# Optimization experiments

Measured on AMD Instinct MI355X. Metric: run time of the kernel, lower is better.

Reference implementation:

```python
import jax, jax.numpy as jnp
import numpy as np

EPS = 1e-9
TEMP = 1.0
TOP_K = 2


def setup_inputs() -> dict:
    key = jax.random.key(0)
    k1, k2, k3, k4 = jax.random.split(key, 4)
    B, T, D, DC, E = 8, 4096, 1024, 512, 64
    din = D + DC
    inputs = jax.random.normal(k1, (B, T, D), dtype=jnp.float32)
    cond = jax.random.normal(k2, (B, T, DC), dtype=jnp.float32)
    # CondRouterMLP params (bias=False): Linear(din -> 2*din), GELU, Linear(2*din -> E)
    W1 = jax.random.normal(k3, (2 * din, din), dtype=jnp.float32) / np.sqrt(din).astype(np.float32)
    W2 = jax.random.normal(k4, (E, 2 * din), dtype=jnp.float32) / np.sqrt(2 * din).astype(np.float32)
    return {"inputs": inputs, "cond": cond, "W1": W1, "W2": W2}


def reference(inputs, cond, W1, W2):
    B, T, D = inputs.shape
    # concat hidden states with condition, flatten tokens
    x = jnp.concatenate([inputs, cond], axis=-1).reshape(-1, D + cond.shape[-1])  # [N, din]
    h = jax.nn.gelu(x @ W1.T, approximate=False)          # [N, 2*din] (torch nn.GELU = exact erf)
    logits = h @ W2.T                                     # [N, E]
    logits = (logits - logits.max(axis=-1, keepdims=True)) / TEMP
    probs = jax.nn.softmax(logits, axis=-1) + EPS
    probs = jnp.clip(probs, EPS, 1.0 - EPS)               # [N, E]
    # eval-mode top-k selection
    top_v, top_i = jax.lax.top_k(probs, TOP_K)            # [N, k]
    N, E = probs.shape
    rows = jnp.arange(N)[:, None]
    router_mask = jnp.zeros_like(probs).at[rows, top_i].set(1.0)
    router_probs = jnp.zeros_like(probs).at[rows, top_i].set(top_v)
    router_probs = router_probs / router_probs.sum(axis=-1, keepdims=True)  # normalize=True
    return (
        router_mask.reshape(B, T, E),
        top_i.reshape(B, T, TOP_K),
        router_probs.reshape(B, T, E),
        probs.reshape(B, T, E),
    )
```

## Files before the change

### kernel.cpp

```cpp
#include <hip/hip_runtime.h>
#include <cmath>

#define N_TOK 32768
#define D0    1024
#define DCC   512
#define DIN   1536
#define JD    3072
#define NE    64
#define BM    128
#define BJ    256
#define BK    32
#define NJC   (JD/BJ)
#define NIT   (DIN/BK)
#define NTH   512
#define HS    36
#define EPSV  1e-9f

typedef _Float16 half8 __attribute__((ext_vector_type(8)));
typedef float    f32x4 __attribute__((ext_vector_type(4)));

#define SZ_A  16384
#define SZ_B  32768
#define OFF_A 0
#define OFF_B 32768
#define LDS_TOTAL 98304
#define OFF_H    0
#define OFF_LRED 0
#define OFF_EPI  36864

#define W1T_G (192*3072)
#define W2T_G (384*64)

__device__ __forceinline__ f32x4 mfma16(half8 a, half8 b, f32x4 c) {
    return __builtin_amdgcn_mfma_f32_16x16x32_f16(a, b, c, 0, 0, 0);
}

__device__ __forceinline__ void split8(const float4 v0, const float4 v1, half8& hh, half8& hl) {
    float f[8] = {v0.x, v0.y, v0.z, v0.w, v1.x, v1.y, v1.z, v1.w};
    #pragma unroll
    for (int i = 0; i < 8; ++i) {
        _Float16 h = (_Float16)f[i];
        hh[i] = h;
        hl[i] = (_Float16)(f[i] - (float)h);
    }
}

__device__ __forceinline__ void gload16(const void* g, void* l) {
    __builtin_amdgcn_global_load_lds(
        (const __attribute__((address_space(1))) unsigned int*)g,
        (__attribute__((address_space(3))) unsigned int*)l, 16, 0, 0);
}

__global__ void presplit_w1t(const float* __restrict__ W1,
                             _Float16* __restrict__ hi, _Float16* __restrict__ lo) {
    int g = blockIdx.x * blockDim.x + threadIdx.x;
    if (g >= W1T_G) return;
    const int j  = g % JD;
    const int ko = g / JD;
    const float* src = W1 + (size_t)j * DIN + ko * 8;
    float4 v0 = *(const float4*)src;
    float4 v1 = *(const float4*)(src + 4);
    half8 h, l;
    split8(v0, v1, h, l);
    *(half8*)(hi + (size_t)g * 8) = h;
    *(half8*)(lo + (size_t)g * 8) = l;
}

__global__ void presplit_w2t(const float* __restrict__ W2,
                             _Float16* __restrict__ hi, _Float16* __restrict__ lo) {
    int g = blockIdx.x * blockDim.x + threadIdx.x;
    if (g >= W2T_G) return;
    const int e  = g & 63;
    const int jo = g >> 6;
    const float* src = W2 + (size_t)e * JD + jo * 8;
    float4 v0 = *(const float4*)src;
    float4 v1 = *(const float4*)(src + 4);
    half8 h, l;
    split8(v0, v1, h, l);
    *(half8*)(hi + (size_t)g * 8) = h;
    *(half8*)(lo + (size_t)g * 8) = l;
}

__global__ __launch_bounds__(NTH, 1)
void router_v9(const float* __restrict__ inp, const float* __restrict__ cnd,
               const _Float16* __restrict__ W1h, const _Float16* __restrict__ W1l,
               const _Float16* __restrict__ W2h, const _Float16* __restrict__ W2l,
               float* __restrict__ out_mask, float* __restrict__ out_topi,
               float* __restrict__ out_rp, float* __restrict__ out_probs)
{
    __shared__ __align__(16) char smem[LDS_TOTAL];

    const int tid  = threadIdx.x;
    const int lane = tid & 63;
    const int w    = tid >> 6;
    const int tg   = w >> 2;
    const int jg   = w & 3;
    const int l15  = lane & 15;
    const int lg   = lane >> 4;
    const int t0   = blockIdx.x * BM;

    const int akoct = w >> 1;
    const int arow  = (w & 1) * 64 + lane;
    const int bplane = w >> 2;
    const int bkoct  = w & 3;

    int aoff[4], boff[4];
    #pragma unroll
    for (int tf = 0; tf < 4; ++tf) aoff[tf] = (lg*128 + tg*64 + tf*16 + l15) * 16;
    #pragma unroll
    for (int jf = 0; jf < 4; ++jf) boff[jf] = (lg*256 + jg*64 + jf*16 + l15) * 16;

    const f32x4 vzero = {0.f, 0.f, 0.f, 0.f};
    f32x4 lacc[4] = {vzero, vzero, vzero, vzero};

    const float* const xrowA = inp + (size_t)(t0 + arow) * D0;
    const float* const xrowC = cnd + (size_t)(t0 + arow) * DCC;
    const _Float16* const Wbp = bplane ? W1l : W1h;

    _Float16* const myHh = (_Float16*)(smem + OFF_H + w * 9216);
    _Float16* const myHl = myHh + 2304;

    for (int jc = 0; jc < NJC; ++jc) {
        f32x4 acc1[4][4];
        #pragma unroll
        for (int tf = 0; tf < 4; ++tf)
            #pragma unroll
            for (int jf = 0; jf < 4; ++jf) acc1[tf][jf] = vzero;

        {
            #pragma unroll
            for (int q = 0; q < 4; ++q) {
                const _Float16* src = Wbp + ((size_t)bkoct * JD + jc*BJ + q*64 + lane) * 8;
                char* dst = smem + OFF_B + bplane*16384 + bkoct*4096 + q*1024;
                gload16(src, dst);
            }
            const float* sx = xrowA + akoct * 8;
            float4 v0 = *(const float4*)sx;
            float4 v1 = *(const float4*)(sx + 4);
            half8 hh, hl;
            split8(v0, v1, hh, hl);
            const int g = (akoct*128 + arow) * 16;
            *(half8*)(smem + OFF_A + g) = hh;
            *(half8*)(smem + OFF_A + 8192 + g) = hl;
        }
        __syncthreads();

        for (int it = 0; it < NIT; ++it) {
            const int cur = it & 1, nxt = cur ^ 1;
            const bool more = (it + 1 < NIT);
            float4 xv0, xv1;
            if (more) {
                const int ko = (it + 1) * 4 + bkoct;
                #pragma unroll
                for (int q = 0; q < 4; ++q) {
                    const _Float16* src = Wbp + ((size_t)ko * JD + jc*BJ + q*64 + lane) * 8;
                    char* dst = smem + OFF_B + nxt*SZ_B + bplane*16384 + bkoct*4096 + q*1024;
                    gload16(src, dst);
                }
                const int k = (it + 1) * BK + akoct * 8;
                const float* sx = (k < D0) ? (xrowA + k) : (xrowC + k - D0);
                xv0 = *(const float4*)sx;
                xv1 = *(const float4*)(sx + 4);
            }
            const char* ab = smem + OFF_A + cur*SZ_A;
            const char* bb = smem + OFF_B + cur*SZ_B;
            half8 ah[4], al[4], bh[4], bl[4];
            #pragma unroll
            for (int tf = 0; tf < 4; ++tf) {
                ah[tf] = *(const half8*)(ab + aoff[tf]);
                al[tf] = *(const half8*)(ab + 8192 + aoff[tf]);
            }
            #pragma unroll
            for (int jf = 0; jf < 4; ++jf) {
                bh[jf] = *(const half8*)(bb + boff[jf]);
                bl[jf] = *(const half8*)(bb + 16384 + boff[jf]);
            }
            #pragma unroll
            for (int tf = 0; tf < 4; ++tf)
                #pragma unroll
                for (int jf = 0; jf < 4; ++jf) {
                    acc1[tf][jf] = mfma16(ah[tf], bh[jf], acc1[tf][jf]);
                    acc1[tf][jf] = mfma16(ah[tf], bl[jf], acc1[tf][jf]);
                    acc1[tf][jf] = mfma16(al[tf], bh[jf], acc1[tf][jf]);
                }
            if (more) {
                half8 hh, hl;
                split8(xv0, xv1, hh, hl);
                const int g = (akoct*128 + arow) * 16;
                *(half8*)(smem + OFF_A + nxt*SZ_A + g) = hh;
                *(half8*)(smem + OFF_A + nxt*SZ_A + 8192 + g) = hl;
            }
            __syncthreads();
        }

        #pragma unroll
        for (int r = 0; r < 2; ++r) {
            #pragma unroll
            for (int c = 0; c < 2; ++c) {
                const int jf = 2*r + c;
                #pragma unroll
                for (int tf = 0; tf < 4; ++tf)
                    #pragma unroll
                    for (int rr = 0; rr < 4; ++rr) {
                        const float v = acc1[tf][jf][rr];
                        const float gv = 0.5f * v * (1.0f + erff(v * 0.70710678118654752f));
                        const _Float16 gh = (_Float16)gv;
                        const _Float16 gl = (_Float16)(gv - (float)gh);
                        const int o = (tf*16 + lg*4 + rr) * HS + c*16 + l15;
                        myHh[o] = gh; myHl[o] = gl;
                    }
            }
            __syncthreads();
            #pragma unroll
            for (int s = 0; s < 4; ++s) {
                const _Float16* sh = (const _Float16*)(smem + OFF_H + (tg*4 + s) * 9216);
                const _Float16* sl = sh + 2304;
                const int jo = jc*32 + s*8 + r*4 + lg;
                const size_t wg = ((size_t)jo * 64 + jg*16 + l15) * 8;
                half8 b2h = *(const half8*)(W2h + wg);
                half8 b2l = *(const half8*)(W2l + wg);
                #pragma unroll
                for (int tf = 0; tf < 4; ++tf) {
                    const int o = (tf*16 + l15) * HS + lg*8;
                    half8 a2h = *(const half8*)(sh + o);
                    half8 a2l = *(const half8*)(sl + o);
                    lacc[tf] = mfma16(a2h, b2h, lacc[tf]);
                    lacc[tf] = mfma16(a2h, b2l, lacc[tf]);
                    lacc[tf] = mfma16(a2l, b2h, lacc[tf]);
                }
            }
            __syncthreads();
        }
    }

    float* const Lred = (float*)(smem + OFF_LRED);
    #pragma unroll
    for (int tf = 0; tf < 4; ++tf)
        #pragma unroll
        for (int rr = 0; rr < 4; ++rr)
            Lred[(tg*64 + tf*16 + lg*4 + rr) * 68 + jg*16 + l15] = lacc[tf][rr];
    __syncthreads();

    float* const mA   = (float*)(smem + OFF_EPI);
    float* const invA = mA + BM;
    int*   const i1A  = (int*)(invA + BM);
    int*   const i2A  = i1A + BM;
    float* const rp1A = (float*)(i2A + BM);
    float* const rp2A = rp1A + BM;

    if (tid < BM) {
        const float* row = Lred + tid * 68;
        float m = -3.402823466e38f;
        for (int e = 0; e < NE; ++e) m = fmaxf(m, row[e]);
        float s = 0.f, v1 = -3.402823466e38f, v2 = -3.402823466e38f;
        int i1 = 0, i2 = 0;
        for (int e = 0; e < NE; ++e) {
            const float v = row[e];
            s += expf(v - m);
            if (v > v1)      { v2 = v1; i2 = i1; v1 = v; i1 = e; }
            else if (v > v2) { v2 = v; i2 = e; }
        }
        const float inv = 1.f / s;
        const float p1 = fminf(expf(v1 - m) * inv + EPSV, 1.f - EPSV);
        const float p2 = fminf(expf(v2 - m) * inv + EPSV, 1.f - EPSV);
        mA[tid] = m; invA[tid] = inv; i1A[tid] = i1; i2A[tid] = i2;
        const float den = p1 + p2;
        rp1A[tid] = p1 / den; rp2A[tid] = p2 / den;
    }
    __syncthreads();

    for (int idx = tid; idx < BM * NE; idx += NTH) {
        const int r = idx >> 6, e = idx & 63;
        const size_t o = (size_t)(t0 + r) * NE + e;
        const float p = fminf(expf(Lred[r * 68 + e] - mA[r]) * invA[r] + EPSV, 1.f - EPSV);
        const int b1 = (e == i1A[r]), b2 = (e == i2A[r]);
        out_probs[o] = p;
        out_mask[o]  = (b1 | b2) ? 1.f : 0.f;
        out_rp[o]    = b1 ? rp1A[r] : (b2 ? rp2A[r] : 0.f);
    }
    if (tid < BM * 2) {
        const int r = tid >> 1, q = tid & 1;
        out_topi[(size_t)(t0 + r) * 2 + q] = (float)(q ? i2A[r] : i1A[r]);
    }
}

extern "C" void kernel_launch(void* const* d_in, const int* in_sizes, int n_in,
                              void* d_out, int out_size, void* d_ws, size_t ws_size,
                              hipStream_t stream) {
    const float* inp = (const float*)d_in[0];
    const float* cnd = (const float*)d_in[1];
    const float* W1  = (const float*)d_in[2];
    const float* W2  = (const float*)d_in[3];

    float* out = (float*)d_out;
    const size_t NT = (size_t)N_TOK;
    float* out_mask  = out;
    float* out_topi  = out + NT * NE;
    float* out_rp    = out + NT * NE + NT * 2;
    float* out_probs = out + NT * NE + NT * 2 + NT * NE;

    _Float16* W1h = (_Float16*)d_ws;
    _Float16* W1l = W1h + (size_t)W1T_G * 8;
    _Float16* W2h = W1l + (size_t)W1T_G * 8;
    _Float16* W2l = W2h + (size_t)W2T_G * 8;

    hipLaunchKernelGGL(presplit_w1t, dim3((W1T_G + 255) / 256), dim3(256), 0, stream, W1, W1h, W1l);
    hipLaunchKernelGGL(presplit_w2t, dim3((W2T_G + 255) / 256), dim3(256), 0, stream, W2, W2h, W2l);
    hipLaunchKernelGGL(router_v9, dim3(N_TOK / BM), dim3(NTH), 0, stream,
                       inp, cnd, W1h, W1l, W2h, W2l,
                       out_mask, out_topi, out_rp, out_probs);
}
```

Baseline: 1.098 ms.

## Halve token tile, load A fragments directly into registers, pipeline W1 across chunks

Cuts the block to 64 tokens and 4 waves so two blocks can share a CU. Each wave now reads its activation rows straight from global memory into MFMA fragments and splits them to hi/lo fp16 in registers, so the A tile is no longer staged in LDS. The W1 prefetch now runs across j-chunk boundaries, removing the per-chunk prologue sync. The cost is that every W1 tile is re-streamed for half as many tokens, which doubles W1 traffic, and the uncoalesced per-lane row loads of x may raise global load latency.

```diff
diff --git a/kernel.cpp b/kernel.cpp
--- a/kernel.cpp
+++ b/kernel.cpp
@@ -7,26 +7,22 @@
 #define DIN   1536
 #define JD    3072
 #define NE    64
-#define BM    128
+#define BM    64
 #define BJ    256
 #define BK    32
 #define NJC   (JD/BJ)
 #define NIT   (DIN/BK)
-#define NTH   512
-#define HS    36
+#define NTH   256
 #define EPSV  1e-9f
 
 typedef _Float16 half8 __attribute__((ext_vector_type(8)));
 typedef float    f32x4 __attribute__((ext_vector_type(4)));
 
-#define SZ_A  16384
 #define SZ_B  32768
-#define OFF_A 0
-#define OFF_B 32768
-#define LDS_TOTAL 98304
-#define OFF_H    0
+#define LDS_TOTAL 65536
+#define OFF_H 32768
 #define OFF_LRED 0
-#define OFF_EPI  36864
+#define OFF_EPI  18432
 
 #define W1T_G (192*3072)
 #define W2T_G (384*64)
@@ -81,152 +77,153 @@
     *(half8*)(lo + (size_t)g * 8) = l;
 }
 
-__global__ __launch_bounds__(NTH, 1)
-void router_v9(const float* __restrict__ inp, const float* __restrict__ cnd,
-               const _Float16* __restrict__ W1h, const _Float16* __restrict__ W1l,
-               const _Float16* __restrict__ W2h, const _Float16* __restrict__ W2l,
-               float* __restrict__ out_mask, float* __restrict__ out_topi,
-               float* __restrict__ out_rp, float* __restrict__ out_probs)
+__global__ __launch_bounds__(NTH, 2)
+void router_v10(const float* __restrict__ inp, const float* __restrict__ cnd,
+                const _Float16* __restrict__ W1h, const _Float16* __restrict__ W1l,
+                const _Float16* __restrict__ W2h, const _Float16* __restrict__ W2l,
+                float* __restrict__ out_mask, float* __restrict__ out_topi,
+                float* __restrict__ out_rp, float* __restrict__ out_probs)
 {
     __shared__ __align__(16) char smem[LDS_TOTAL];
 
     const int tid  = threadIdx.x;
     const int lane = tid & 63;
     const int w    = tid >> 6;
-    const int tg   = w >> 2;
-    const int jg   = w & 3;
+    const int tg   = w >> 1;
+    const int jg   = w & 1;
     const int l15  = lane & 15;
     const int lg   = lane >> 4;
     const int t0   = blockIdx.x * BM;
 
-    const int akoct = w >> 1;
-    const int arow  = (w & 1) * 64 + lane;
-    const int bplane = w >> 2;
-    const int bkoct  = w & 3;
-
-    int aoff[4], boff[4];
+    const int spl = w >> 1;
+    const int sko = (w & 1) * 2;
+
+    int boff[8];
     #pragma unroll
-    for (int tf = 0; tf < 4; ++tf) aoff[tf] = (lg*128 + tg*64 + tf*16 + l15) * 16;
+    for (int jf = 0; jf < 8; ++jf)
+        boff[jf] = (lg * 256 + jg * 128 + jf * 16 + l15) * 16;
+
+    const float* pA[2];
+    const float* pC[2];
     #pragma unroll
-    for (int jf = 0; jf < 4; ++jf) boff[jf] = (lg*256 + jg*64 + jf*16 + l15) * 16;
+    for (int tf = 0; tf < 2; ++tf) {
+        const int row = t0 + tg * 32 + tf * 16 + l15;
+        pA[tf] = inp + (size_t)row * D0;
+        pC[tf] = cnd + (size_t)row * DCC;
+    }
+
+    _Float16* const myHh = (_Float16*)(smem + OFF_H + w * 4608);
+    _Float16* const myHl = myHh + 1152;
 
     const f32x4 vzero = {0.f, 0.f, 0.f, 0.f};
     f32x4 lacc[4] = {vzero, vzero, vzero, vzero};
 
-    const float* const xrowA = inp + (size_t)(t0 + arow) * D0;
-    const float* const xrowC = cnd + (size_t)(t0 + arow) * DCC;
-    const _Float16* const Wbp = bplane ? W1l : W1h;
-
-    _Float16* const myHh = (_Float16*)(smem + OFF_H + w * 9216);
-    _Float16* const myHl = myHh + 2304;
+    float4 xv[2][2];
+    {
+        #pragma unroll
+        for (int d = 0; d < 2; ++d) {
+            const int ko = sko + d;
+            #pragma unroll
+            for (int q = 0; q < 4; ++q) {
+                const _Float16* src = (spl ? W1l : W1h) +
+                    ((size_t)ko * JD + q * 64 + lane) * 8;
+                gload16(src, smem + ((spl * 4 + ko) * 256 + q * 64) * 16);
+            }
+        }
+        #pragma unroll
+        for (int tf = 0; tf < 2; ++tf) {
+            const float* s = pA[tf] + lg * 8;
+            xv[tf][0] = *(const float4*)s;
+            xv[tf][1] = *(const float4*)(s + 4);
+        }
+    }
+    __syncthreads();
 
     for (int jc = 0; jc < NJC; ++jc) {
-        f32x4 acc1[4][4];
-        #pragma unroll
-        for (int tf = 0; tf < 4; ++tf)
-            #pragma unroll
-            for (int jf = 0; jf < 4; ++jf) acc1[tf][jf] = vzero;
-
-        {
-            #pragma unroll
-            for (int q = 0; q < 4; ++q) {
-                const _Float16* src = Wbp + ((size_t)bkoct * JD + jc*BJ + q*64 + lane) * 8;
-                char* dst = smem + OFF_B + bplane*16384 + bkoct*4096 + q*1024;
-                gload16(src, dst);
-            }
-            const float* sx = xrowA + akoct * 8;
-            float4 v0 = *(const float4*)sx;
-            float4 v1 = *(const float4*)(sx + 4);
-            half8 hh, hl;
-            split8(v0, v1, hh, hl);
-            const int g = (akoct*128 + arow) * 16;
-            *(half8*)(smem + OFF_A + g) = hh;
-            *(half8*)(smem + OFF_A + 8192 + g) = hl;
-        }
-        __syncthreads();
+        f32x4 acc1[2][8];
+        #pragma unroll
+        for (int tf = 0; tf < 2; ++tf)
+            #pragma unroll
+            for (int jf = 0; jf < 8; ++jf) acc1[tf][jf] = vzero;
 
         for (int it = 0; it < NIT; ++it) {
-            const int cur = it & 1, nxt = cur ^ 1;
-            const bool more = (it + 1 < NIT);
-            float4 xv0, xv1;
+            const int cur = it & 1;
+            const bool more = !(jc == NJC - 1 && it == NIT - 1);
+            half8 ah[2], al[2];
+            #pragma unroll
+            for (int tf = 0; tf < 2; ++tf)
+                split8(xv[tf][0], xv[tf][1], ah[tf], al[tf]);
             if (more) {
-                const int ko = (it + 1) * 4 + bkoct;
-                #pragma unroll
-                for (int q = 0; q < 4; ++q) {
-                    const _Float16* src = Wbp + ((size_t)ko * JD + jc*BJ + q*64 + lane) * 8;
-                    char* dst = smem + OFF_B + nxt*SZ_B + bplane*16384 + bkoct*4096 + q*1024;
-                    gload16(src, dst);
+                const int itn = (it == NIT - 1) ? 0 : it + 1;
+                const int jcn = (it == NIT - 1) ? jc + 1 : jc;
+                char* bb = smem + (cur ^ 1) * SZ_B;
+                #pragma unroll
+                for (int d = 0; d < 2; ++d) {
+                    const int ko = sko + d;
+                    const size_t kog = (size_t)(itn * 4 + ko) * JD + jcn * BJ;
+                    #pragma unroll
+                    for (int q = 0; q < 4; ++q) {
+                        const _Float16* src = (spl ? W1l : W1h) + (kog + q * 64 + lane) * 8;
+                        gload16(src, bb + ((spl * 4 + ko) * 256 + q * 64) * 16);
+                    }
                 }
-                const int k = (it + 1) * BK + akoct * 8;
-                const float* sx = (k < D0) ? (xrowA + k) : (xrowC + k - D0);
-                xv0 = *(const float4*)sx;
-                xv1 = *(const float4*)(sx + 4);
-            }
-            const char* ab = smem + OFF_A + cur*SZ_A;
-            const char* bb = smem + OFF_B + cur*SZ_B;
-            half8 ah[4], al[4], bh[4], bl[4];
-            #pragma unroll
-            for (int tf = 0; tf < 4; ++tf) {
-                ah[tf] = *(const half8*)(ab + aoff[tf]);
-                al[tf] = *(const half8*)(ab + 8192 + aoff[tf]);
-            }
-            #pragma unroll
-            for (int jf = 0; jf < 4; ++jf) {
-                bh[jf] = *(const half8*)(bb + boff[jf]);
-                bl[jf] = *(const half8*)(bb + 16384 + boff[jf]);
-            }
-            #pragma unroll
-            for (int tf = 0; tf < 4; ++tf)
-                #pragma unroll
-                for (int jf = 0; jf < 4; ++jf) {
-                    acc1[tf][jf] = mfma16(ah[tf], bh[jf], acc1[tf][jf]);
-                    acc1[tf][jf] = mfma16(ah[tf], bl[jf], acc1[tf][jf]);
-                    acc1[tf][jf] = mfma16(al[tf], bh[jf], acc1[tf][jf]);
+                const int k0 = itn * BK + lg * 8;
+                #pragma unroll
+                for (int tf = 0; tf < 2; ++tf) {
+                    const float* s = (itn < 32) ? (pA[tf] + k0) : (pC[tf] + k0 - D0);
+                    xv[tf][0] = *(const float4*)s;
+                    xv[tf][1] = *(const float4*)(s + 4);
                 }
-            if (more) {
-                half8 hh, hl;
-                split8(xv0, xv1, hh, hl);
-                const int g = (akoct*128 + arow) * 16;
-                *(half8*)(smem + OFF_A + nxt*SZ_A + g) = hh;
-                *(half8*)(smem + OFF_A + nxt*SZ_A + 8192 + g) = hl;
+            }
+            const char* bb = smem + cur * SZ_B;
+            #pragma unroll
+            for (int jf = 0; jf < 8; ++jf) {
+                half8 bh = *(const half8*)(bb + boff[jf]);
+                half8 bl = *(const half8*)(bb + 16384 + boff[jf]);
+                #pragma unroll
+                for (int tf = 0; tf < 2; ++tf) {
+                    acc1[tf][jf] = mfma16(ah[tf], bh, acc1[tf][jf]);
+                    acc1[tf][jf] = mfma16(ah[tf], bl, acc1[tf][jf]);
+                    acc1[tf][jf] = mfma16(al[tf], bh, acc1[tf][jf]);
+                }
             }
             __syncthreads();
         }
 
         #pragma unroll
-        for (int r = 0; r < 2; ++r) {
+        for (int r = 0; r < 4; ++r) {
             #pragma unroll
             for (int c = 0; c < 2; ++c) {
-                const int jf = 2*r + c;
-                #pragma unroll
-                for (int tf = 0; tf < 4; ++tf)
+                const int jf = 2 * r + c;
+                #pragma unroll
+                for (int tf = 0; tf < 2; ++tf)
                     #pragma unroll
                     for (int rr = 0; rr < 4; ++rr) {
                         const float v = acc1[tf][jf][rr];
                         const float gv = 0.5f * v * (1.0f + erff(v * 0.70710678118654752f));
                         const _Float16 gh = (_Float16)gv;
                         const _Float16 gl = (_Float16)(gv - (float)gh);
-                        const int o = (tf*16 + lg*4 + rr) * HS + c*16 + l15;
+                        const int o = (tf * 16 + lg * 4 + rr) * 36 + c * 16 + l15;
                         myHh[o] = gh; myHl[o] = gl;
                     }
             }
             __syncthreads();
             #pragma unroll
-            for (int s = 0; s < 4; ++s) {
-                const _Float16* sh = (const _Float16*)(smem + OFF_H + (tg*4 + s) * 9216);
-                const _Float16* sl = sh + 2304;
-                const int jo = jc*32 + s*8 + r*4 + lg;
-                const size_t wg = ((size_t)jo * 64 + jg*16 + l15) * 8;
+            for (int jg2 = 0; jg2 < 2; ++jg2) {
+                const int jo = jc * 32 + jg2 * 16 + r * 4 + lg;
+                const size_t wg = ((size_t)jo * 64 + w * 16 + l15) * 8;
                 half8 b2h = *(const half8*)(W2h + wg);
                 half8 b2l = *(const half8*)(W2l + wg);
                 #pragma unroll
-                for (int tf = 0; tf < 4; ++tf) {
-                    const int o = (tf*16 + l15) * HS + lg*8;
+                for (int tf2 = 0; tf2 < 4; ++tf2) {
+                    const _Float16* sh = (const _Float16*)(smem + OFF_H + ((tf2 >> 1) * 2 + jg2) * 4608);
+                    const _Float16* sl = sh + 1152;
+                    const int o = ((tf2 & 1) * 16 + l15) * 36 + lg * 8;
                     half8 a2h = *(const half8*)(sh + o);
                     half8 a2l = *(const half8*)(sl + o);
-                    lacc[tf] = mfma16(a2h, b2h, lacc[tf]);
-                    lacc[tf] = mfma16(a2h, b2l, lacc[tf]);
-                    lacc[tf] = mfma16(a2l, b2h, lacc[tf]);
+                    lacc[tf2] = mfma16(a2h, b2h, lacc[tf2]);
+                    lacc[tf2] = mfma16(a2h, b2l, lacc[tf2]);
+                    lacc[tf2] = mfma16(a2l, b2h, lacc[tf2]);
                 }
             }
             __syncthreads();
@@ -235,10 +232,10 @@
 
     float* const Lred = (float*)(smem + OFF_LRED);
     #pragma unroll
-    for (int tf = 0; tf < 4; ++tf)
+    for (int tf2 = 0; tf2 < 4; ++tf2)
         #pragma unroll
         for (int rr = 0; rr < 4; ++rr)
-            Lred[(tg*64 + tf*16 + lg*4 + rr) * 68 + jg*16 + l15] = lacc[tf][rr];
+            Lred[(tf2 * 16 + lg * 4 + rr) * 68 + w * 16 + l15] = lacc[tf2][rr];
     __syncthreads();
 
     float* const mA   = (float*)(smem + OFF_EPI);
@@ -306,7 +303,7 @@
 
     hipLaunchKernelGGL(presplit_w1t, dim3((W1T_G + 255) / 256), dim3(256), 0, stream, W1, W1h, W1l);
     hipLaunchKernelGGL(presplit_w2t, dim3((W2T_G + 255) / 256), dim3(256), 0, stream, W2, W2h, W2l);
-    hipLaunchKernelGGL(router_v9, dim3(N_TOK / BM), dim3(NTH), 0, stream,
+    hipLaunchKernelGGL(router_v10, dim3(N_TOK / BM), dim3(NTH), 0, stream,
                        inp, cnd, W1h, W1l, W2h, W2l,
                        out_mask, out_topi, out_rp, out_probs);
 }
```

Measured after the change: 1.246 ms. +13.5%, slower.

## Triple-buffer W1 tiles with prefetch distance two and lighter barriers

Applied to the files above, without the earlier changes.

Moves the W1 hi/lo tiles from double to triple buffering in LDS. Global-to-LDS loads are now issued two k-steps ahead, and the prologue preloads two tiles. The per-iteration __syncthreads is replaced by a barrier that waits only on LDS counters, not on global memory counters, so weight loads can stay in flight across iterations and hide memory latency behind the MFMA work. In exchange LDS use grows to 128 KB and the H scratch region is moved. Since the barrier no longer waits on outstanding global-to-LDS transfers, a tile could be read before its load has fully landed.

```diff
diff --git a/kernel.cpp b/kernel.cpp
--- a/kernel.cpp
+++ b/kernel.cpp
@@ -23,8 +23,8 @@
 #define SZ_B  32768
 #define OFF_A 0
 #define OFF_B 32768
-#define LDS_TOTAL 98304
-#define OFF_H    0
+#define LDS_TOTAL 131072
+#define OFF_H    32768
 #define OFF_LRED 0
 #define OFF_EPI  36864
 
@@ -50,6 +50,11 @@
         (const __attribute__((address_space(1))) unsigned int*)g,
         (__attribute__((address_space(3))) unsigned int*)l, 16, 0, 0);
 }
+
+#define SOFT_BARRIER() do { \
+    asm volatile("s_waitcnt lgkmcnt(0)" ::: "memory"); \
+    __builtin_amdgcn_s_barrier(); \
+} while (0)
 
 __global__ void presplit_w1t(const float* __restrict__ W1,
                              _Float16* __restrict__ hi, _Float16* __restrict__ lo) {
@@ -82,11 +87,11 @@
 }
 
 __global__ __launch_bounds__(NTH, 1)
-void router_v9(const float* __restrict__ inp, const float* __restrict__ cnd,
-               const _Float16* __restrict__ W1h, const _Float16* __restrict__ W1l,
-               const _Float16* __restrict__ W2h, const _Float16* __restrict__ W2l,
-               float* __restrict__ out_mask, float* __restrict__ out_topi,
-               float* __restrict__ out_rp, float* __restrict__ out_probs)
+void router_v11(const float* __restrict__ inp, const float* __restrict__ cnd,
+                const _Float16* __restrict__ W1h, const _Float16* __restrict__ W1l,
+                const _Float16* __restrict__ W2h, const _Float16* __restrict__ W2l,
+                float* __restrict__ out_mask, float* __restrict__ out_topi,
+                float* __restrict__ out_rp, float* __restrict__ out_probs)
 {
     __shared__ __align__(16) char smem[LDS_TOTAL];
 
@@ -128,42 +133,48 @@
             for (int jf = 0; jf < 4; ++jf) acc1[tf][jf] = vzero;
 
         {
-            #pragma unroll
-            for (int q = 0; q < 4; ++q) {
-                const _Float16* src = Wbp + ((size_t)bkoct * JD + jc*BJ + q*64 + lane) * 8;
-                char* dst = smem + OFF_B + bplane*16384 + bkoct*4096 + q*1024;
-                gload16(src, dst);
-            }
-            const float* sx = xrowA + akoct * 8;
-            float4 v0 = *(const float4*)sx;
-            float4 v1 = *(const float4*)(sx + 4);
+            float4 v0 = *(const float4*)(xrowA + akoct * 8);
+            float4 v1 = *(const float4*)(xrowA + akoct * 8 + 4);
+            #pragma unroll
+            for (int d = 0; d < 2; ++d) {
+                const int ko = d * 4 + bkoct;
+                const _Float16* src = Wbp + ((size_t)ko * JD + jc * BJ) * 8;
+                char* dst = smem + OFF_B + d * SZ_B + (bplane * 4 + bkoct) * 4096;
+                #pragma unroll
+                for (int q = 0; q < 4; ++q)
+                    gload16(src + (size_t)(q * 64 + lane) * 8, dst + q * 1024);
+            }
             half8 hh, hl;
             split8(v0, v1, hh, hl);
-            const int g = (akoct*128 + arow) * 16;
+            const int g = (akoct * 128 + arow) * 16;
             *(half8*)(smem + OFF_A + g) = hh;
             *(half8*)(smem + OFF_A + 8192 + g) = hl;
+            asm volatile("s_waitcnt vmcnt(0) lgkmcnt(0)" ::: "memory");
+            __builtin_amdgcn_s_barrier();
         }
-        __syncthreads();
 
         for (int it = 0; it < NIT; ++it) {
-            const int cur = it & 1, nxt = cur ^ 1;
-            const bool more = (it + 1 < NIT);
+            const bool haveA = (it + 1 < NIT);
+            const bool haveB = (it + 2 < NIT);
             float4 xv0, xv1;
-            if (more) {
-                const int ko = (it + 1) * 4 + bkoct;
-                #pragma unroll
-                for (int q = 0; q < 4; ++q) {
-                    const _Float16* src = Wbp + ((size_t)ko * JD + jc*BJ + q*64 + lane) * 8;
-                    char* dst = smem + OFF_B + nxt*SZ_B + bplane*16384 + bkoct*4096 + q*1024;
-                    gload16(src, dst);
-                }
+            if (haveA) {
                 const int k = (it + 1) * BK + akoct * 8;
                 const float* sx = (k < D0) ? (xrowA + k) : (xrowC + k - D0);
                 xv0 = *(const float4*)sx;
                 xv1 = *(const float4*)(sx + 4);
-            }
-            const char* ab = smem + OFF_A + cur*SZ_A;
-            const char* bb = smem + OFF_B + cur*SZ_B;
+                __builtin_amdgcn_sched_barrier(0);
+            }
+            if (haveB) {
+                const int ko = (it + 2) * 4 + bkoct;
+                const _Float16* src = Wbp + ((size_t)ko * JD + jc * BJ) * 8;
+                char* dst = smem + OFF_B + ((it + 2) % 3) * SZ_B
+                          + (bplane * 4 + bkoct) * 4096;
+                #pragma unroll
+                for (int q = 0; q < 4; ++q)
+                    gload16(src + (size_t)(q * 64 + lane) * 8, dst + q * 1024);
+            }
+            const char* ab = smem + OFF_A + (it & 1) * SZ_A;
+            const char* bb = smem + OFF_B + (it % 3) * SZ_B;
             half8 ah[4], al[4], bh[4], bl[4];
             #pragma unroll
             for (int tf = 0; tf < 4; ++tf) {
@@ -183,14 +194,19 @@
                     acc1[tf][jf] = mfma16(ah[tf], bl[jf], acc1[tf][jf]);
                     acc1[tf][jf] = mfma16(al[tf], bh[jf], acc1[tf][jf]);
                 }
-            if (more) {
+            if (haveA) {
                 half8 hh, hl;
                 split8(xv0, xv1, hh, hl);
-                const int g = (akoct*128 + arow) * 16;
-                *(half8*)(smem + OFF_A + nxt*SZ_A + g) = hh;
-                *(half8*)(smem + OFF_A + nxt*SZ_A + 8192 + g) = hl;
-            }
-            __syncthreads();
+                char* nab = smem + OFF_A + ((it + 1) & 1) * SZ_A;
+                const int g = (akoct * 128 + arow) * 16;
+                *(half8*)(nab + g) = hh;
+                *(half8*)(nab + 8192 + g) = hl;
+            }
+            if (it < NIT - 1) {
+                SOFT_BARRIER();
+            } else {
+                __syncthreads();
+            }
         }
 
         #pragma unroll
@@ -306,7 +322,7 @@
 
     hipLaunchKernelGGL(presplit_w1t, dim3((W1T_G + 255) / 256), dim3(256), 0, stream, W1, W1h, W1l);
     hipLaunchKernelGGL(presplit_w2t, dim3((W2T_G + 255) / 256), dim3(256), 0, stream, W2, W2h, W2l);
-    hipLaunchKernelGGL(router_v9, dim3(N_TOK / BM), dim3(NTH), 0, stream,
+    hipLaunchKernelGGL(router_v11, dim3(N_TOK / BM), dim3(NTH), 0, stream,
                        inp, cnd, W1h, W1l, W2h, W2l,
                        out_mask, out_topi, out_rp, out_probs);
 }
```

Result: slower. 1.228 ms (+11.8%).

## Load activations directly into MFMA registers and double K-step to 64

Applied to the files above, without the earlier changes.

Drops the LDS staging of the split activation tile. Each lane now loads its own fp32 activation fragments from global memory straight into registers and splits them to hi/lo halves in place. K per iteration doubles to 64, which halves the number of barriers, and the weight double buffer grows to fill 128KB of LDS. This removes LDS writes and reads for A. In exchange, each row's activations are loaded redundantly by the four column-group waves, register pressure rises, and global load latency is less hidden because loads are issued in the same iteration they are used.

```diff
diff --git a/kernel.cpp b/kernel.cpp
--- a/kernel.cpp
+++ b/kernel.cpp
@@ -9,7 +9,7 @@
 #define NE    64
 #define BM    128
 #define BJ    256
-#define BK    32
+#define BK    64
 #define NJC   (JD/BJ)
 #define NIT   (DIN/BK)
 #define NTH   512
@@ -19,11 +19,8 @@
 typedef _Float16 half8 __attribute__((ext_vector_type(8)));
 typedef float    f32x4 __attribute__((ext_vector_type(4)));
 
-#define SZ_A  16384
-#define SZ_B  32768
-#define OFF_A 0
-#define OFF_B 32768
-#define LDS_TOTAL 98304
+#define SZ_B  65536
+#define LDS_TOTAL 131072
 #define OFF_H    0
 #define OFF_LRED 0
 #define OFF_EPI  36864
@@ -82,11 +79,11 @@
 }
 
 __global__ __launch_bounds__(NTH, 1)
-void router_v9(const float* __restrict__ inp, const float* __restrict__ cnd,
-               const _Float16* __restrict__ W1h, const _Float16* __restrict__ W1l,
-               const _Float16* __restrict__ W2h, const _Float16* __restrict__ W2l,
-               float* __restrict__ out_mask, float* __restrict__ out_topi,
-               float* __restrict__ out_rp, float* __restrict__ out_probs)
+void router_v14(const float* __restrict__ inp, const float* __restrict__ cnd,
+                const _Float16* __restrict__ W1h, const _Float16* __restrict__ W1l,
+                const _Float16* __restrict__ W2h, const _Float16* __restrict__ W2l,
+                float* __restrict__ out_mask, float* __restrict__ out_topi,
+                float* __restrict__ out_rp, float* __restrict__ out_probs)
 {
     __shared__ __align__(16) char smem[LDS_TOTAL];
 
@@ -99,23 +96,27 @@
     const int lg   = lane >> 4;
     const int t0   = blockIdx.x * BM;
 
-    const int akoct = w >> 1;
-    const int arow  = (w & 1) * 64 + lane;
-    const int bplane = w >> 2;
-    const int bkoct  = w & 3;
-
-    int aoff[4], boff[4];
+    const int bpl = w >> 2;
+    const int kp  = (w & 3) * 2;
+
+    int boff[4];
     #pragma unroll
-    for (int tf = 0; tf < 4; ++tf) aoff[tf] = (lg*128 + tg*64 + tf*16 + l15) * 16;
+    for (int jf = 0; jf < 4; ++jf)
+        boff[jf] = (lg * 256 + jg * 64 + jf * 16 + l15) * 16;
+
+    const float* pI[4];
+    const float* pC[4];
     #pragma unroll
-    for (int jf = 0; jf < 4; ++jf) boff[jf] = (lg*256 + jg*64 + jf*16 + l15) * 16;
+    for (int tf = 0; tf < 4; ++tf) {
+        const int row = t0 + tg * 64 + tf * 16 + l15;
+        pI[tf] = inp + (size_t)row * D0;
+        pC[tf] = cnd + (size_t)row * DCC;
+    }
 
     const f32x4 vzero = {0.f, 0.f, 0.f, 0.f};
     f32x4 lacc[4] = {vzero, vzero, vzero, vzero};
 
-    const float* const xrowA = inp + (size_t)(t0 + arow) * D0;
-    const float* const xrowC = cnd + (size_t)(t0 + arow) * DCC;
-    const _Float16* const Wbp = bplane ? W1l : W1h;
+    const _Float16* const Wbp = bpl ? W1l : W1h;
 
     _Float16* const myHh = (_Float16*)(smem + OFF_H + w * 9216);
     _Float16* const myHl = myHh + 2304;
@@ -129,66 +130,88 @@
 
         {
             #pragma unroll
-            for (int q = 0; q < 4; ++q) {
-                const _Float16* src = Wbp + ((size_t)bkoct * JD + jc*BJ + q*64 + lane) * 8;
-                char* dst = smem + OFF_B + bplane*16384 + bkoct*4096 + q*1024;
-                gload16(src, dst);
-            }
-            const float* sx = xrowA + akoct * 8;
-            float4 v0 = *(const float4*)sx;
-            float4 v1 = *(const float4*)(sx + 4);
-            half8 hh, hl;
-            split8(v0, v1, hh, hl);
-            const int g = (akoct*128 + arow) * 16;
-            *(half8*)(smem + OFF_A + g) = hh;
-            *(half8*)(smem + OFF_A + 8192 + g) = hl;
+            for (int d = 0; d < 2; ++d) {
+                const int koct = kp + d;
+                const _Float16* src = Wbp + ((size_t)koct * JD + jc * BJ) * 8;
+                char* dst = smem + ((bpl * 8 + koct) * 256) * 16;
+                #pragma unroll
+                for (int q = 0; q < 4; ++q)
+                    gload16(src + (size_t)(q * 64 + lane) * 8, dst + q * 1024);
+            }
         }
         __syncthreads();
 
         for (int it = 0; it < NIT; ++it) {
-            const int cur = it & 1, nxt = cur ^ 1;
+            const int cur = it & 1;
             const bool more = (it + 1 < NIT);
-            float4 xv0, xv1;
+
+            float4 xa[4][2], xb[4][2];
+            const int k0 = it * BK + lg * 8;
+            const int k1 = k0 + 32;
+            #pragma unroll
+            for (int tf = 0; tf < 4; ++tf) {
+                const float* s0 = (k0 < D0) ? (pI[tf] + k0) : (pC[tf] + k0 - D0);
+                xa[tf][0] = *(const float4*)s0;
+                xa[tf][1] = *(const float4*)(s0 + 4);
+            }
+            #pragma unroll
+            for (int tf = 0; tf < 4; ++tf) {
+                const float* s1 = (k1 < D0) ? (pI[tf] + k1) : (pC[tf] + k1 - D0);
+                xb[tf][0] = *(const float4*)s1;
+                xb[tf][1] = *(const float4*)(s1 + 4);
+            }
+            __builtin_amdgcn_sched_barrier(0);
+
             if (more) {
-                const int ko = (it + 1) * 4 + bkoct;
-                #pragma unroll
-                for (int q = 0; q < 4; ++q) {
-                    const _Float16* src = Wbp + ((size_t)ko * JD + jc*BJ + q*64 + lane) * 8;
-                    char* dst = smem + OFF_B + nxt*SZ_B + bplane*16384 + bkoct*4096 + q*1024;
-                    gload16(src, dst);
+                char* bb = smem + (cur ^ 1) * SZ_B;
+                #pragma unroll
+                for (int d = 0; d < 2; ++d) {
+                    const int koct = kp + d;
+                    const _Float16* src = Wbp +
+                        ((size_t)((it + 1) * 8 + koct) * JD + jc * BJ) * 8;
+                    char* dst = bb + ((bpl * 8 + koct) * 256) * 16;
+                    #pragma unroll
+                    for (int q = 0; q < 4; ++q)
+                        gload16(src + (size_t)(q * 64 + lane) * 8, dst + q * 1024);
                 }
-                const int k = (it + 1) * BK + akoct * 8;
-                const float* sx = (k < D0) ? (xrowA + k) : (xrowC + k - D0);
-                xv0 = *(const float4*)sx;
-                xv1 = *(const float4*)(sx + 4);
-            }
-            const char* ab = smem + OFF_A + cur*SZ_A;
-            const char* bb = smem + OFF_B + cur*SZ_B;
-            half8 ah[4], al[4], bh[4], bl[4];
-            #pragma unroll
-            for (int tf = 0; tf < 4; ++tf) {
-                ah[tf] = *(const half8*)(ab + aoff[tf]);
-                al[tf] = *(const half8*)(ab + 8192 + aoff[tf]);
-            }
-            #pragma unroll
-            for (int jf = 0; jf < 4; ++jf) {
-                bh[jf] = *(const half8*)(bb + boff[jf]);
-                bl[jf] = *(const half8*)(bb + 16384 + boff[jf]);
-            }
-            #pragma unroll
-            for (int tf = 0; tf < 4; ++tf)
+            }
+
+            const char* bb = smem + cur * SZ_B;
+            {
+                half8 ah[4], al[4], bh[4], bl[4];
                 #pragma unroll
                 for (int jf = 0; jf < 4; ++jf) {
-                    acc1[tf][jf] = mfma16(ah[tf], bh[jf], acc1[tf][jf]);
-                    acc1[tf][jf] = mfma16(ah[tf], bl[jf], acc1[tf][jf]);
-                    acc1[tf][jf] = mfma16(al[tf], bh[jf], acc1[tf][jf]);
+                    bh[jf] = *(const half8*)(bb + boff[jf]);
+                    bl[jf] = *(const half8*)(bb + boff[jf] + 32768);
                 }
-            if (more) {
-                half8 hh, hl;
-                split8(xv0, xv1, hh, hl);
-                const int g = (akoct*128 + arow) * 16;
-                *(half8*)(smem + OFF_A + nxt*SZ_A + g) = hh;
-                *(half8*)(smem + OFF_A + nxt*SZ_A + 8192 + g) = hl;
+                #pragma unroll
+                for (int tf = 0; tf < 4; ++tf) split8(xa[tf][0], xa[tf][1], ah[tf], al[tf]);
+                #pragma unroll
+                for (int tf = 0; tf < 4; ++tf)
+                    #pragma unroll
+                    for (int jf = 0; jf < 4; ++jf) {
+                        acc1[tf][jf] = mfma16(ah[tf], bh[jf], acc1[tf][jf]);
+                        acc1[tf][jf] = mfma16(ah[tf], bl[jf], acc1[tf][jf]);
+                        acc1[tf][jf] = mfma16(al[tf], bh[jf], acc1[tf][jf]);
+                    }
+            }
+            {
+                half8 ah[4], al[4], bh[4], bl[4];
+                #pragma unroll
+                for (int jf = 0; jf < 4; ++jf) {
+                    bh[jf] = *(const half8*)(bb + boff[jf] + 16384);
+                    bl[jf] = *(const half8*)(bb + boff[jf] + 16384 + 32768);
+                }
+                #pragma unroll
+                for (int tf = 0; tf < 4; ++tf) split8(xb[tf][0], xb[tf][1], ah[tf], al[tf]);
+                #pragma unroll
+                for (int tf = 0; tf < 4; ++tf)
+                    #pragma unroll
+                    for (int jf = 0; jf < 4; ++jf) {
+                        acc1[tf][jf] = mfma16(ah[tf], bh[jf], acc1[tf][jf]);
+                        acc1[tf][jf] = mfma16(ah[tf], bl[jf], acc1[tf][jf]);
+                        acc1[tf][jf] = mfma16(al[tf], bh[jf], acc1[tf][jf]);
+                    }
             }
             __syncthreads();
         }
@@ -306,7 +329,7 @@
 
     hipLaunchKernelGGL(presplit_w1t, dim3((W1T_G + 255) / 256), dim3(256), 0, stream, W1, W1h, W1l);
     hipLaunchKernelGGL(presplit_w2t, dim3((W2T_G + 255) / 256), dim3(256), 0, stream, W2, W2h, W2l);
-    hipLaunchKernelGGL(router_v9, dim3(N_TOK / BM), dim3(NTH), 0, stream,
+    hipLaunchKernelGGL(router_v14, dim3(N_TOK / BM), dim3(NTH), 0, stream,
                        inp, cnd, W1h, W1l, W2h, W2l,
                        out_mask, out_topi, out_rp, out_probs);
 }
```

Result: slower. 1.708 ms (+55.6%).
